# Optimization experiments

Measured on AMD Instinct MI355X. Metric: run time of the kernel, lower is better.

The kernel has to match this reference:

```python
import jax, jax.numpy as jnp
import numpy as np

E_IN = 1 << 20   # input events
E_OUT = 1 << 17  # output events (= len(times_out))
K = 9            # kernel_size (temporal taps)
C_IN = 64        # filters_in
C_OUT = 64       # filters


def setup_inputs() -> dict:
    key = jax.random.key(0)
    ks = jax.random.split(key, 6)
    features = jax.random.normal(ks[0], (E_IN, C_IN), jnp.float32)
    dt = jax.random.uniform(ks[1], (E_IN,), jnp.float32)          # time since event, >= 0
    times_out = jax.random.uniform(ks[2], (E_OUT,), jnp.float32)  # only its length is used
    successor_kernel_ids = jax.random.randint(ks[3], (E_IN,), 0, K, jnp.int32)
    segment_ids_out = jax.random.randint(ks[4], (E_IN,), 0, E_OUT, jnp.int32)
    # parameters per build(): decay_rate (C_in,) zeros-init, kernel glorot, bias zeros
    decay_rate = jnp.zeros((C_IN,), jnp.float32)
    glorot = float(np.sqrt(2.0 / (C_IN + C_OUT)))
    kernel = jax.random.normal(ks[5], (K, C_IN, C_OUT), jnp.float32) * glorot
    bias = jnp.zeros((C_OUT,), jnp.float32)
    return dict(features=features, dt=dt, times_out=times_out,
                decay_rate=decay_rate, kernel=kernel, bias=bias,
                successor_kernel_ids=successor_kernel_ids,
                segment_ids_out=segment_ids_out)


def reference(features, dt, times_out, decay_rate, kernel, bias,
              successor_kernel_ids, segment_ids_out):
    """ExclusiveConv forward: exp-decay weighting, per-kernel-tap segment sum,
    normalization by summed decay weights, small kernel matmul, bias.
    normalize=True, activation=None, decay_rate_activation=softplus."""
    k, c_in, c_out = kernel.shape
    e_out = times_out.shape[0]
    rate = jax.nn.softplus(decay_rate)                       # [C_in]
    w = jnp.exp(-dt[:, None] * rate[None, :])                # [E_in, C_in] decay weights
    vals = w * features                                      # [E_in, C_in]
    # each input event goes exclusively to (output event, kernel tap)
    seg = segment_ids_out.astype(jnp.int32) * k + successor_kernel_ids  # [E_in]
    num = jax.ops.segment_sum(vals, seg, num_segments=e_out * k)        # [E_out*K, C_in]
    den = jax.ops.segment_sum(w, seg, num_segments=e_out * k)           # [E_out*K, C_in]
    agg = jnp.where(den > 0, num / jnp.where(den > 0, den, 1.0), 0.0)   # normalized
    agg = agg.reshape(e_out, k, c_in)
    out = jnp.einsum('ekc,kcf->ef', agg, kernel) + bias      # [E_out, C_out]
    return out
```

## Files before the change

kernel.cpp:

```cpp
#include <hip/hip_runtime.h>
#include <hip/hip_bf16.h>
#include <stdint.h>

#define E_IN_N   1048576
#define E_OUT_N  131072
#define KTAPS    9
#define CIN      64
#define COUT     64
#define NCELL    (E_OUT_N*KTAPS)
#define NB_SCAN  1152
#define TILE_E   32
#define NKSTEP   18
#define CHUNK    32

typedef __attribute__((ext_vector_type(8))) short bf16x8;
typedef __attribute__((ext_vector_type(4))) float f32x4;

__device__ __forceinline__ ushort f32_bf16(float x){
  union{float f; uint32_t u;} v; v.f=x;
  uint32_t r = v.u + 0x7FFFu + ((v.u>>16)&1u);
  return (ushort)(r>>16);
}

__global__ void prep_k(int* __restrict__ counts, const float* __restrict__ wk,
                       ushort* __restrict__ wb){
  int b=blockIdx.x, t=threadIdx.x;
  if(b<1152){
    ((int4*)counts)[b*256+t]=int4{0,0,0,0};
  }else{
    int slot=(b-1152)*256+t;
    int j=slot&7; int t2=slot>>3; int lane=t2&63; int t3=t2>>6;
    int ks=t3%NKSTEP; int nt=t3/NKSTEP;
    int r=ks*32+((lane>>4)*8)+j; int col=nt*16+(lane&15);
    wb[slot]=f32_bf16(wk[r*COUT+col]);
  }
}

__global__ void hist_k(const int* __restrict__ seg, const int* __restrict__ succ,
                       int* __restrict__ counts, uint32_t* __restrict__ cellrank){
  int i = blockIdx.x*256 + threadIdx.x;
  uint32_t cell = (uint32_t)(seg[i]*KTAPS + succ[i]);
  uint32_t rank = (uint32_t)atomicAdd(&counts[cell],1);
  cellrank[i] = (cell<<11) | rank;
}

__global__ void blocksum_k(const int* __restrict__ counts, int* __restrict__ bsum){
  __shared__ int sm[256];
  int b=blockIdx.x, t=threadIdx.x;
  const int4 c4 = *(const int4*)(counts + b*1024 + t*4);
  int s=c4.x+c4.y+c4.z+c4.w;
  sm[t]=s; __syncthreads();
  for(int d=128; d>0; d>>=1){ if(t<d) sm[t]+=sm[t+d]; __syncthreads(); }
  if(t==0) bsum[b]=sm[0];
}

__global__ void offsets_k(const int* __restrict__ counts, const int* __restrict__ bsum,
                          int* __restrict__ offsets){
  __shared__ int sm[256];
  int b=blockIdx.x, t=threadIdx.x;
  int s=0;
  for(int j=t; j<NB_SCAN; j+=256) if(j<b) s+=bsum[j];
  sm[t]=s; __syncthreads();
  for(int d=128; d>0; d>>=1){ if(t<d) sm[t]+=sm[t+d]; __syncthreads(); }
  int base0=sm[0]; __syncthreads();
  int base=b*1024+t*4;
  const int4 c4=*(const int4*)(counts+base);
  int s2=c4.x+c4.y+c4.z+c4.w;
  sm[t]=s2; __syncthreads();
  for(int d=1; d<256; d<<=1){ int x=(t>=d)?sm[t-d]:0; __syncthreads(); sm[t]+=x; __syncthreads(); }
  int e0v=base0 + ((t==0)?0:sm[t-1]);
  int4 o; o.x=e0v; o.y=e0v+c4.x; o.z=o.y+c4.y; o.w=o.z+c4.z;
  *(int4*)(offsets+base)=o;
  if(b==NB_SCAN-1 && t==255) offsets[NCELL]=o.w+c4.w;
}

__global__ void scatter_k(const uint32_t* __restrict__ cellrank, const float* __restrict__ dtv,
                          const int* __restrict__ offsets, int2* __restrict__ sorted2){
  int i=blockIdx.x*256+threadIdx.x;
  uint32_t cr=cellrank[i];
  uint32_t cell=cr>>11, rank=cr&2047u;
  int base=offsets[cell];
  float d=dtv[i];
  uint32_t x=cell>>5;
  uint32_t q=__umulhi(x,477218592u);
  uint32_t rel=cell - q*288u;
  sorted2[base+(int)rank]=int2{(int)((uint32_t)i | (rel<<20)), __float_as_int(d)};
}

__global__ __launch_bounds__(512,4) void compute_k(
    const float* __restrict__ features, const float* __restrict__ decay,
    const float* __restrict__ bias, const int* __restrict__ offsets,
    const int2* __restrict__ sorted2, const ushort* __restrict__ wb,
    float* __restrict__ out)
{
  __shared__ ushort agg[TILE_E*584];
  const int tid=threadIdx.x, wv=tid>>6, lane=tid&63;
  const int e0=blockIdx.x*TILE_E;
  const int cb0=e0*KTAPS;

  for(int i=tid;i<TILE_E*584/2;i+=512) ((uint32_t*)agg)[i]=0u;
  float x=decay[lane];
  float rate=fmaxf(x,0.f)+log1pf(__expf(-fabsf(x)));
  __syncthreads();

  {
    const int c0=cb0+wv*36;
    int jv=0; if(lane<2) jv=offsets[c0+lane*36];
    int cb = __builtin_amdgcn_readfirstlane(__shfl(jv,0));
    const int jE = __builtin_amdgcn_readfirstlane(__shfl(jv,1));

    int prevRel=-1;
    float num=0.f, den=1.f;

    while(cb<jE){
      int qx[CHUNK]; float qd[CHUNK];
      #pragma unroll
      for(int e=0;e<CHUNK;e++){
        int2 t=sorted2[cb+e];
        qx[e]=t.x; qd[e]=__int_as_float(t.y);
      }
      float fl[CHUNK];
      #pragma unroll
      for(int e=0;e<CHUNK;e++){
        int iu = qx[e] & 0xFFFFF;
        fl[e] = features[((size_t)iu<<6) + lane];
      }
      #pragma unroll
      for(int e=0;e<CHUNK;e++){
        const int ok = (cb+e) < jE;
        int rel = (int)(((uint32_t)qx[e])>>20);
        rel = ok ? rel : prevRel;
        float w = __expf(-qd[e]*rate);
        w = ok ? w : 0.f;
        const float same = (rel==prevRel) ? 1.f : 0.f;
        num = num*same + w*fl[e];
        den = den*same + w;
        const int le=(rel*7282)>>16, kk=rel-le*9;
        agg[le*584 + kk*64 + lane] = f32_bf16(num*__builtin_amdgcn_rcpf(den));
        prevRel = rel;
      }
      cb += CHUNK;
    }
  }
  __syncthreads();

  const int mt=wv>>2, nt=wv&3;
  const int arow=mt*16+(lane&15);
  const int koff=(lane>>4)*8;
  const ushort* wbp = wb + ((size_t)(nt*NKSTEP)*64 + (size_t)lane)*8;
  f32x4 acc={0.f,0.f,0.f,0.f};
  #pragma unroll
  for(int ks=0;ks<NKSTEP;ks++){
    bf16x8 a=*(const bf16x8*)&agg[arow*584+ks*32+koff];
    bf16x8 bfr=*(const bf16x8*)(wbp + (size_t)ks*512);
    acc=__builtin_amdgcn_mfma_f32_16x16x32_bf16(a,bfr,acc,0,0,0);
  }
  const int orow=e0+mt*16+((lane>>4)*4);
  const int ocol=nt*16+(lane&15);
  const float bv=bias[ocol];
  #pragma unroll
  for(int r=0;r<4;r++) out[(size_t)(orow+r)*COUT+ocol]=acc[r]+bv;
}

extern "C" void kernel_launch(void* const* d_in, const int* in_sizes, int n_in,
                              void* d_out, int out_size, void* d_ws, size_t ws_size,
                              hipStream_t stream){
  const float* features=(const float*)d_in[0];
  const float* dtv=(const float*)d_in[1];
  const float* decay=(const float*)d_in[3];
  const float* wk=(const float*)d_in[4];
  const float* bias=(const float*)d_in[5];
  const int* succ=(const int*)d_in[6];
  const int* seg=(const int*)d_in[7];

  char* ws=(char*)d_ws;
  size_t o=0;
  int* counts=(int*)(ws+o);      o+=(size_t)NCELL*4;
  int* offsets=(int*)(ws+o);     o+=(size_t)(NCELL+4)*4;
  int* bsum=(int*)(ws+o);        o+=(size_t)NB_SCAN*4;
  uint32_t* cellrank=(uint32_t*)(ws+o); o+=(size_t)E_IN_N*4;
  int2* sorted2=(int2*)(ws+o);   o+=(size_t)(E_IN_N+CHUNK)*8;
  ushort* wb=(ushort*)(ws+o);    o+=(size_t)36864*2;
  float* out=(float*)d_out;

  hipLaunchKernelGGL(prep_k, dim3(1296),dim3(256),0,stream, counts,wk,wb);
  hipLaunchKernelGGL(hist_k, dim3(E_IN_N/256),dim3(256),0,stream, seg,succ,counts,cellrank);
  hipLaunchKernelGGL(blocksum_k, dim3(NB_SCAN),dim3(256),0,stream, counts,bsum);
  hipLaunchKernelGGL(offsets_k, dim3(NB_SCAN),dim3(256),0,stream, counts,bsum,offsets);
  hipLaunchKernelGGL(scatter_k, dim3(E_IN_N/256),dim3(256),0,stream, cellrank,dtv,offsets,sorted2);
  hipLaunchKernelGGL(compute_k, dim3(E_OUT_N/TILE_E),dim3(512),0,stream,
                     features,decay,bias,offsets,sorted2,wb,out);
}
```

Measured before the change: 185.2 us.

## Scatter bf16-packed feature rows into sorted order before compute

The scatter kernel now copies each input event's feature row, converted to bf16, into a sorted buffer. The compute kernel then reads features contiguously in segment order instead of gathering random 256-byte rows. This replaces the random gather with a coalesced streaming read and halves the feature bytes read in compute. The cost is an extra scattered write of the whole feature matrix and added bf16 rounding of the inputs. CHUNK is also reduced from 32 to 16.

```diff
diff --git a/kernel.cpp b/kernel.cpp
--- a/kernel.cpp
+++ b/kernel.cpp
@@ -11,7 +11,7 @@
 #define NB_SCAN  1152
 #define TILE_E   32
 #define NKSTEP   18
-#define CHUNK    32
+#define CHUNK    16
 
 typedef __attribute__((ext_vector_type(8))) short bf16x8;
 typedef __attribute__((ext_vector_type(4))) float f32x4;
@@ -74,23 +74,29 @@
   if(b==NB_SCAN-1 && t==255) offsets[NCELL]=o.w+c4.w;
 }
 
-__global__ void scatter_k(const uint32_t* __restrict__ cellrank, const float* __restrict__ dtv,
-                          const int* __restrict__ offsets, int2* __restrict__ sorted2){
-  int i=blockIdx.x*256+threadIdx.x;
-  uint32_t cr=cellrank[i];
-  uint32_t cell=cr>>11, rank=cr&2047u;
-  int base=offsets[cell];
-  float d=dtv[i];
-  uint32_t x=cell>>5;
-  uint32_t q=__umulhi(x,477218592u);
-  uint32_t rel=cell - q*288u;
-  sorted2[base+(int)rank]=int2{(int)((uint32_t)i | (rel<<20)), __float_as_int(d)};
+__global__ void scatterF_k(const float* __restrict__ features, const float* __restrict__ dtv,
+                           const uint32_t* __restrict__ cellrank, const int* __restrict__ offsets,
+                           uint32_t* __restrict__ sortedF, int2* __restrict__ sorted2){
+  const int r = blockIdx.x*8 + (threadIdx.x>>5);
+  const int l = threadIdx.x&31;
+  uint32_t cr = cellrank[r];
+  uint32_t cell = cr>>11, rank = cr&2047u;
+  int pos = offsets[cell] + (int)rank;
+  float2 f2 = *(const float2*)(features + ((size_t)r<<6) + 2*l);
+  uint32_t packed = ((uint32_t)f32_bf16(f2.y)<<16) | (uint32_t)f32_bf16(f2.x);
+  sortedF[((size_t)pos<<5) + l] = packed;
+  if(l==0){
+    uint32_t x=cell>>5;
+    uint32_t q=__umulhi(x,477218592u);
+    uint32_t rel=cell - q*288u;
+    sorted2[pos]=int2{(int)(rel<<20), __float_as_int(dtv[r])};
+  }
 }
 
 __global__ __launch_bounds__(512,4) void compute_k(
-    const float* __restrict__ features, const float* __restrict__ decay,
-    const float* __restrict__ bias, const int* __restrict__ offsets,
-    const int2* __restrict__ sorted2, const ushort* __restrict__ wb,
+    const float* __restrict__ decay, const float* __restrict__ bias,
+    const int* __restrict__ offsets, const int2* __restrict__ sorted2,
+    const ushort* __restrict__ sortedF, const ushort* __restrict__ wb,
     float* __restrict__ out)
 {
   __shared__ ushort agg[TILE_E*584];
@@ -119,12 +125,10 @@
         int2 t=sorted2[cb+e];
         qx[e]=t.x; qd[e]=__int_as_float(t.y);
       }
-      float fl[CHUNK];
+      ushort us[CHUNK];
       #pragma unroll
-      for(int e=0;e<CHUNK;e++){
-        int iu = qx[e] & 0xFFFFF;
-        fl[e] = features[((size_t)iu<<6) + lane];
-      }
+      for(int e=0;e<CHUNK;e++)
+        us[e]=sortedF[((size_t)(cb+e)<<6) + lane];
       #pragma unroll
       for(int e=0;e<CHUNK;e++){
         const int ok = (cb+e) < jE;
@@ -132,8 +136,9 @@
         rel = ok ? rel : prevRel;
         float w = __expf(-qd[e]*rate);
         w = ok ? w : 0.f;
+        float f = __uint_as_float(((uint32_t)us[e])<<16);
         const float same = (rel==prevRel) ? 1.f : 0.f;
-        num = num*same + w*fl[e];
+        num = num*same + w*f;
         den = den*same + w;
         const int le=(rel*7282)>>16, kk=rel-le*9;
         agg[le*584 + kk*64 + lane] = f32_bf16(num*__builtin_amdgcn_rcpf(den));
@@ -180,6 +185,7 @@
   int* bsum=(int*)(ws+o);        o+=(size_t)NB_SCAN*4;
   uint32_t* cellrank=(uint32_t*)(ws+o); o+=(size_t)E_IN_N*4;
   int2* sorted2=(int2*)(ws+o);   o+=(size_t)(E_IN_N+CHUNK)*8;
+  uint32_t* sortedF=(uint32_t*)(ws+o); o+=(size_t)(E_IN_N+CHUNK)*128;
   ushort* wb=(ushort*)(ws+o);    o+=(size_t)36864*2;
   float* out=(float*)d_out;
 
@@ -187,7 +193,8 @@
   hipLaunchKernelGGL(hist_k, dim3(E_IN_N/256),dim3(256),0,stream, seg,succ,counts,cellrank);
   hipLaunchKernelGGL(blocksum_k, dim3(NB_SCAN),dim3(256),0,stream, counts,bsum);
   hipLaunchKernelGGL(offsets_k, dim3(NB_SCAN),dim3(256),0,stream, counts,bsum,offsets);
-  hipLaunchKernelGGL(scatter_k, dim3(E_IN_N/256),dim3(256),0,stream, cellrank,dtv,offsets,sorted2);
+  hipLaunchKernelGGL(scatterF_k, dim3(E_IN_N/8),dim3(256),0,stream,
+                     features,dtv,cellrank,offsets,sortedF,sorted2);
   hipLaunchKernelGGL(compute_k, dim3(E_OUT_N/TILE_E),dim3(512),0,stream,
-                     features,decay,bias,offsets,sorted2,wb,out);
-}
+                     decay,bias,offsets,sorted2,(const ushort*)sortedF,wb,out);
+}
```

Measured after the change: 289.7 us. 1.56x slower.

## Convert features to bf16 in histogram pass to halve gather bytes

Applied to the files above, without the earlier changes.

The histogram kernel now also streams the full fp32 feature matrix and writes a bf16 copy to workspace. The compute kernel gathers 2-byte features instead of 4-byte ones, cutting the bytes moved by the random per-event gather. The chunk size is reduced from 32 to 16, and the rel field is masked to 9 bits. In exchange the full features array is read and written in bf16 once more (256 MB read, 128 MB written), and input precision drops to bf16 before weighting.

```diff
diff --git a/kernel.cpp b/kernel.cpp
--- a/kernel.cpp
+++ b/kernel.cpp
@@ -11,7 +11,7 @@
 #define NB_SCAN  1152
 #define TILE_E   32
 #define NKSTEP   18
-#define CHUNK    32
+#define CHUNK    16
 
 typedef __attribute__((ext_vector_type(8))) short bf16x8;
 typedef __attribute__((ext_vector_type(4))) float f32x4;
@@ -36,12 +36,21 @@
   }
 }
 
-__global__ void hist_k(const int* __restrict__ seg, const int* __restrict__ succ,
-                       int* __restrict__ counts, uint32_t* __restrict__ cellrank){
-  int i = blockIdx.x*256 + threadIdx.x;
+__global__ void histcvt_k(const int* __restrict__ seg, const int* __restrict__ succ,
+                          int* __restrict__ counts, uint32_t* __restrict__ cellrank,
+                          const float* __restrict__ features, uint32_t* __restrict__ featB){
+  int b=blockIdx.x, t=threadIdx.x;
+  int i = b*256 + t;
   uint32_t cell = (uint32_t)(seg[i]*KTAPS + succ[i]);
   uint32_t rank = (uint32_t)atomicAdd(&counts[cell],1);
   cellrank[i] = (cell<<11) | rank;
+  const float2* src = (const float2*)(features + ((size_t)b<<14));
+  uint32_t* dst = featB + ((size_t)b<<13);
+  #pragma unroll
+  for(int k=0;k<32;k++){
+    float2 f2 = src[k*256 + t];
+    dst[k*256 + t] = ((uint32_t)f32_bf16(f2.y)<<16) | (uint32_t)f32_bf16(f2.x);
+  }
 }
 
 __global__ void blocksum_k(const int* __restrict__ counts, int* __restrict__ bsum){
@@ -88,9 +97,9 @@
 }
 
 __global__ __launch_bounds__(512,4) void compute_k(
-    const float* __restrict__ features, const float* __restrict__ decay,
-    const float* __restrict__ bias, const int* __restrict__ offsets,
-    const int2* __restrict__ sorted2, const ushort* __restrict__ wb,
+    const float* __restrict__ decay, const float* __restrict__ bias,
+    const int* __restrict__ offsets, const int2* __restrict__ sorted2,
+    const ushort* __restrict__ featB, const ushort* __restrict__ wb,
     float* __restrict__ out)
 {
   __shared__ ushort agg[TILE_E*584];
@@ -119,21 +128,22 @@
         int2 t=sorted2[cb+e];
         qx[e]=t.x; qd[e]=__int_as_float(t.y);
       }
-      float fl[CHUNK];
+      ushort us[CHUNK];
       #pragma unroll
       for(int e=0;e<CHUNK;e++){
         int iu = qx[e] & 0xFFFFF;
-        fl[e] = features[((size_t)iu<<6) + lane];
+        us[e] = featB[((size_t)iu<<6) + lane];
       }
       #pragma unroll
       for(int e=0;e<CHUNK;e++){
         const int ok = (cb+e) < jE;
-        int rel = (int)(((uint32_t)qx[e])>>20);
+        int rel = (int)(((uint32_t)qx[e])>>20) & 511;
         rel = ok ? rel : prevRel;
         float w = __expf(-qd[e]*rate);
         w = ok ? w : 0.f;
+        float f = __uint_as_float(((uint32_t)us[e])<<16);
         const float same = (rel==prevRel) ? 1.f : 0.f;
-        num = num*same + w*fl[e];
+        num = num*same + w*f;
         den = den*same + w;
         const int le=(rel*7282)>>16, kk=rel-le*9;
         agg[le*584 + kk*64 + lane] = f32_bf16(num*__builtin_amdgcn_rcpf(den));
@@ -180,14 +190,16 @@
   int* bsum=(int*)(ws+o);        o+=(size_t)NB_SCAN*4;
   uint32_t* cellrank=(uint32_t*)(ws+o); o+=(size_t)E_IN_N*4;
   int2* sorted2=(int2*)(ws+o);   o+=(size_t)(E_IN_N+CHUNK)*8;
+  uint32_t* featB=(uint32_t*)(ws+o); o+=(size_t)E_IN_N*128 + 4096;
   ushort* wb=(ushort*)(ws+o);    o+=(size_t)36864*2;
   float* out=(float*)d_out;
 
   hipLaunchKernelGGL(prep_k, dim3(1296),dim3(256),0,stream, counts,wk,wb);
-  hipLaunchKernelGGL(hist_k, dim3(E_IN_N/256),dim3(256),0,stream, seg,succ,counts,cellrank);
+  hipLaunchKernelGGL(histcvt_k, dim3(E_IN_N/256),dim3(256),0,stream,
+                     seg,succ,counts,cellrank,features,featB);
   hipLaunchKernelGGL(blocksum_k, dim3(NB_SCAN),dim3(256),0,stream, counts,bsum);
   hipLaunchKernelGGL(offsets_k, dim3(NB_SCAN),dim3(256),0,stream, counts,bsum,offsets);
   hipLaunchKernelGGL(scatter_k, dim3(E_IN_N/256),dim3(256),0,stream, cellrank,dtv,offsets,sorted2);
   hipLaunchKernelGGL(compute_k, dim3(E_OUT_N/TILE_E),dim3(512),0,stream,
-                     features,decay,bias,offsets,sorted2,wb,out);
-}
+                     decay,bias,offsets,sorted2,(const ushort*)featB,wb,out);
+}
```

Result: slower. 206.3 us (+11.4%).

## Double-buffer event gathers in compute kernel to overlap loads with consumption

Applied to the files above, without the earlier changes.

The per-wave segment loop becomes a two-stage software pipeline with chunks of 16. The feature gather for the next chunk and the index/dt load for the one after are issued before the current chunk's decay-weighted accumulation runs, so memory latency can overlap with ALU work. A sched_barrier stops the compiler from moving the gathers past that point. Register pressure rises from holding two buffers, and the padding of the sorted buffer grows to cover the extra read-ahead.

```diff
diff --git a/kernel.cpp b/kernel.cpp
--- a/kernel.cpp
+++ b/kernel.cpp
@@ -11,7 +11,7 @@
 #define NB_SCAN  1152
 #define TILE_E   32
 #define NKSTEP   18
-#define CHUNK    32
+#define CHUNK    16
 
 typedef __attribute__((ext_vector_type(8))) short bf16x8;
 typedef __attribute__((ext_vector_type(4))) float f32x4;
@@ -87,6 +87,31 @@
   sorted2[base+(int)rank]=int2{(int)((uint32_t)i | (rel<<20)), __float_as_int(d)};
 }
 
+#define LOADP(QX,QD,BASE) { \
+  _Pragma("unroll") \
+  for(int e=0;e<CHUNK;e++){ int2 t=sorted2[(BASE)+e]; QX[e]=t.x; QD[e]=__int_as_float(t.y); } }
+
+#define GATHER(FL,QX) { \
+  _Pragma("unroll") \
+  for(int e=0;e<CHUNK;e++){ int iu=QX[e]&0xFFFFF; FL[e]=features[((size_t)iu<<6)+lane]; } \
+  __builtin_amdgcn_sched_barrier(0); }
+
+#define CONSUME(FL,QX,QD,BASE) { \
+  _Pragma("unroll") \
+  for(int e=0;e<CHUNK;e++){ \
+    const int ok=(BASE)+e<jE; \
+    int rel=(int)(((uint32_t)QX[e])>>20); \
+    rel = ok?rel:prevRel; \
+    float w=__expf(-QD[e]*rate); \
+    w = ok?w:0.f; \
+    const float same=(rel==prevRel)?1.f:0.f; \
+    num=num*same+w*FL[e]; \
+    den=den*same+w; \
+    const int le=(rel*7282)>>16, kk=rel-le*9; \
+    agg[le*584+kk*64+lane]=f32_bf16(num*__builtin_amdgcn_rcpf(den)); \
+    prevRel=rel; \
+  } }
+
 __global__ __launch_bounds__(512,4) void compute_k(
     const float* __restrict__ features, const float* __restrict__ decay,
     const float* __restrict__ bias, const int* __restrict__ offsets,
@@ -112,34 +137,22 @@
     int prevRel=-1;
     float num=0.f, den=1.f;
 
-    while(cb<jE){
-      int qx[CHUNK]; float qd[CHUNK];
-      #pragma unroll
-      for(int e=0;e<CHUNK;e++){
-        int2 t=sorted2[cb+e];
-        qx[e]=t.x; qd[e]=__int_as_float(t.y);
+    if(cb<jE){
+      int xA[CHUNK]; float dA[CHUNK]; float fA[CHUNK];
+      int xB[CHUNK]; float dB[CHUNK]; float fB[CHUNK];
+      LOADP(xA,dA,cb)
+      GATHER(fA,xA)
+      LOADP(xB,dB,cb+CHUNK)
+      while(true){
+        GATHER(fB,xB)
+        CONSUME(fA,xA,dA,cb)
+        cb+=CHUNK; if(cb>=jE) break;
+        LOADP(xA,dA,cb+CHUNK)
+        GATHER(fA,xA)
+        CONSUME(fB,xB,dB,cb)
+        cb+=CHUNK; if(cb>=jE) break;
+        LOADP(xB,dB,cb+CHUNK)
       }
-      float fl[CHUNK];
-      #pragma unroll
-      for(int e=0;e<CHUNK;e++){
-        int iu = qx[e] & 0xFFFFF;
-        fl[e] = features[((size_t)iu<<6) + lane];
-      }
-      #pragma unroll
-      for(int e=0;e<CHUNK;e++){
-        const int ok = (cb+e) < jE;
-        int rel = (int)(((uint32_t)qx[e])>>20);
-        rel = ok ? rel : prevRel;
-        float w = __expf(-qd[e]*rate);
-        w = ok ? w : 0.f;
-        const float same = (rel==prevRel) ? 1.f : 0.f;
-        num = num*same + w*fl[e];
-        den = den*same + w;
-        const int le=(rel*7282)>>16, kk=rel-le*9;
-        agg[le*584 + kk*64 + lane] = f32_bf16(num*__builtin_amdgcn_rcpf(den));
-        prevRel = rel;
-      }
-      cb += CHUNK;
     }
   }
   __syncthreads();
@@ -179,7 +192,7 @@
   int* offsets=(int*)(ws+o);     o+=(size_t)(NCELL+4)*4;
   int* bsum=(int*)(ws+o);        o+=(size_t)NB_SCAN*4;
   uint32_t* cellrank=(uint32_t*)(ws+o); o+=(size_t)E_IN_N*4;
-  int2* sorted2=(int2*)(ws+o);   o+=(size_t)(E_IN_N+CHUNK)*8;
+  int2* sorted2=(int2*)(ws+o);   o+=(size_t)(E_IN_N+64)*8;
   ushort* wb=(ushort*)(ws+o);    o+=(size_t)36864*2;
   float* out=(float*)d_out;
 
```

Result: no change. 184.5 us (-0.4%).
